# Kernel optimization log

Measured on AMD Instinct MI355X. Metric: run time of the kernel, lower is better.

The kernel has to match this reference:

```python
import jax, jax.numpy as jnp
import numpy as np

DIM = 512

def setup_inputs() -> dict:
    key = jax.random.key(0)
    k1, k2, k3 = jax.random.split(key, 3)
    context = jax.random.normal(k1, (64, 1024, DIM), dtype=jnp.float32)
    query = jax.random.normal(k2, (64, 128, DIM), dtype=jnp.float32)
    # nn.Linear(3*dim, 1, bias=False) weight, flattened to a (3*dim,) vector
    w0 = jax.random.normal(k3, (3 * DIM,), dtype=jnp.float32) * (1.0 / np.sqrt(3 * DIM))
    return {"context": context, "query": query, "w0": w0}

def reference(context, query, w0):
    # Trilinear similarity: sim[b,i,j] = w_c.c_i + w_q.q_j + w_m.(c_i*q_j)
    # (equivalent to Linear(concat([c, q, c*q])) without materializing the concat)
    d = context.shape[-1]
    wc, wq, wm = w0[:d], w0[d:2 * d], w0[2 * d:]
    sim = (context @ wc)[:, :, None] \
        + (query @ wq)[:, None, :] \
        + jnp.einsum('bid,bjd->bij', context * wm, query)  # (B, ctx, q)
    # Original: softmax over trailing dim of size 1 -> all ones (faithful to the bug)
    S = jnp.ones_like(sim)                 # (B, ctx, q)
    SS = jax.nn.softmax(sim, axis=1)       # softmax over context dim
    A = S @ query                          # (B, ctx, d)
    B = S @ jnp.swapaxes(SS, 1, 2) @ context  # (B, ctx, d)
    return (A, B)
```

## Files before the change

### kernel.cpp

```cpp
#include <hip/hip_runtime.h>
#include <hip/hip_bf16.h>

#define NB   64
#define NC   1024
#define NQ   128
#define DIMD 512
#define BK   64
#define NKC  (DIMD / BK)
#define LDK  (BK + 8)
#define TM   128
#define NTILE (NC / TM)

using short8  = __attribute__((ext_vector_type(8))) short;
using short4v = __attribute__((ext_vector_type(4))) short;
using f32x4   = __attribute__((ext_vector_type(4))) float;
typedef __fp16 half2v __attribute__((ext_vector_type(2)));

__device__ inline float dot4(float4 a, float4 b) {
    return a.x * b.x + a.y * b.y + a.z * b.z + a.w * b.w;
}

__global__ __launch_bounds__(256) void gemm_stats(
    const float* __restrict__ ctx, const float* __restrict__ qry,
    const float* __restrict__ w0, float* __restrict__ stats,
    unsigned short* __restrict__ eh)
{
    __shared__ __attribute__((aligned(16))) short As[TM][LDK];
    __shared__ __attribute__((aligned(16))) short Bs[NQ][LDK];
    __shared__ __attribute__((aligned(16))) float w0L[3 * DIMD];
    __shared__ float cwL[TM], qwL[NQ];
    __shared__ float sL[2][NQ];

    const int tid  = threadIdx.x;
    const int b    = blockIdx.x;
    const int bt   = blockIdx.y;
    const int i0   = bt * TM;
    const int w    = tid >> 6;
    const int lane = tid & 63;
    const int wr   = w >> 1, wcg = w & 1;
    const int RB   = wr * 64, CB = wcg * 64;
    const int n16  = lane & 15, qd = lane >> 4;

    for (int idx = tid; idx < 3 * DIMD; idx += 256) w0L[idx] = w0[idx];

    f32x4 acc[4][4];
#pragma unroll
    for (int ri = 0; ri < 4; ri++)
#pragma unroll
        for (int ci = 0; ci < 4; ci++)
#pragma unroll
            for (int e = 0; e < 4; e++) acc[ri][ci][e] = 0.f;

    const int col4  = n16 * 4;
    const int srow0 = w * 32 + qd;
    const float* cBase = ctx + ((size_t)(b * NC + i0 + srow0)) * DIMD + col4;
    const float* qBase = qry + ((size_t)(b * NQ + srow0)) * DIMD + col4;
    float cwp[8], qwp[8];
#pragma unroll
    for (int u = 0; u < 8; u++) { cwp[u] = 0.f; qwp[u] = 0.f; }

    for (int kc = 0; kc < NKC; kc++) {
        const int k0 = kc * BK;
        __syncthreads();
        float4 wcv = *(const float4*)&w0L[k0 + col4];
        float4 wqv = *(const float4*)&w0L[DIMD + k0 + col4];
        float4 wmv = *(const float4*)&w0L[2 * DIMD + k0 + col4];
#pragma unroll
        for (int u = 0; u < 8; u++) {
            const int row = w * 32 + u * 4 + qd;
            float4 v = *(const float4*)(cBase + k0 + (size_t)u * 4 * DIMD);
            cwp[u] += dot4(v, wcv);
            union { __hip_bfloat162 h[2]; short4v s; } pc;
            pc.h[0] = __float22bfloat162_rn(make_float2(v.x * wmv.x, v.y * wmv.y));
            pc.h[1] = __float22bfloat162_rn(make_float2(v.z * wmv.z, v.w * wmv.w));
            *(short4v*)&As[row][col4] = pc.s;

            float4 q = *(const float4*)(qBase + k0 + (size_t)u * 4 * DIMD);
            qwp[u] += dot4(q, wqv);
            union { __hip_bfloat162 h[2]; short4v s; } pq;
            pq.h[0] = __float22bfloat162_rn(make_float2(q.x, q.y));
            pq.h[1] = __float22bfloat162_rn(make_float2(q.z, q.w));
            *(short4v*)&Bs[row][col4] = pq.s;
        }
        __syncthreads();
#pragma unroll
        for (int ks = 0; ks < BK / 32; ks++) {
            const int kb = ks * 32 + qd * 8;
            short8 af[4], bfr[4];
#pragma unroll
            for (int ri = 0; ri < 4; ri++) af[ri] = *(const short8*)&As[RB + ri * 16 + n16][kb];
#pragma unroll
            for (int ci = 0; ci < 4; ci++) bfr[ci] = *(const short8*)&Bs[CB + ci * 16 + n16][kb];
#pragma unroll
            for (int ri = 0; ri < 4; ri++)
#pragma unroll
                for (int ci = 0; ci < 4; ci++)
                    acc[ri][ci] = __builtin_amdgcn_mfma_f32_16x16x32_bf16(
                        af[ri], bfr[ci], acc[ri][ci], 0, 0, 0);
        }
    }

#pragma unroll
    for (int u = 0; u < 8; u++) {
        float c = cwp[u], q = qwp[u];
#pragma unroll
        for (int off = 1; off < 16; off <<= 1) {
            c += __shfl_xor(c, off);
            q += __shfl_xor(q, off);
        }
        if (n16 == 0) {
            const int row = w * 32 + u * 4 + qd;
            cwL[row] = c; qwL[row] = q;
        }
    }
    __syncthreads();

#pragma unroll
    for (int ci = 0; ci < 4; ci++) {
        const int col = CB + ci * 16 + n16;
        const float qwv = qwL[col];
        unsigned short* eCol = eh + ((size_t)(b * NTILE + bt) * NQ + col) * TM;
        float s = 0.f;
#pragma unroll
        for (int ri = 0; ri < 4; ri++) {
            const int rbase = RB + ri * 16 + qd * 4;
            float e0 = __expf(acc[ri][ci][0] + cwL[rbase + 0] + qwv);
            float e1 = __expf(acc[ri][ci][1] + cwL[rbase + 1] + qwv);
            float e2 = __expf(acc[ri][ci][2] + cwL[rbase + 2] + qwv);
            float e3 = __expf(acc[ri][ci][3] + cwL[rbase + 3] + qwv);
            half2v h01 = __builtin_amdgcn_cvt_pkrtz(e0, e1);
            half2v h23 = __builtin_amdgcn_cvt_pkrtz(e2, e3);
            s += (float)h01[0] + (float)h01[1] + (float)h23[0] + (float)h23[1];
            uint2 pk;
            pk.x = __builtin_bit_cast(unsigned, h01);
            pk.y = __builtin_bit_cast(unsigned, h23);
            *(uint2*)&eCol[rbase] = pk;
        }
        s += __shfl_xor(s, 16);
        s += __shfl_xor(s, 32);
        if (qd == 0) sL[wr][col] = s;
    }
    __syncthreads();
    if (tid < NQ)
        stats[(size_t)(b * NTILE + bt) * NQ + tid] = sL[0][tid] + sL[1][tid];
}

__global__ __launch_bounds__(256) void rb2(
    const float* __restrict__ ctx, const float* __restrict__ qry,
    const unsigned short* __restrict__ eh, const float* __restrict__ stats,
    float* __restrict__ bpart, float* __restrict__ arow)
{
    __shared__ __attribute__((aligned(16))) unsigned short eL[NQ * TM];
    __shared__ float izL[NQ];
    __shared__ float rpart[2][TM];
    __shared__ float rfin[TM];
    __shared__ float qL[4][64];

    const int tid = threadIdx.x;
    const int b = blockIdx.x, bt = blockIdx.y;
    const int i0 = bt * TM;

    if (tid < NQ) {
        float ssum = 0.f;
#pragma unroll
        for (int t8 = 0; t8 < NTILE; t8++)
            ssum += stats[(size_t)(b * NTILE + t8) * NQ + tid];
        izL[tid] = 1.0f / ssum;
    }
    const unsigned short* tileSrc = eh + (size_t)(b * NTILE + bt) * NQ * TM;
#pragma unroll
    for (int it = 0; it < 8; it++) {
        const int idx = (tid + it * 256) * 8;
        *(uint4*)&eL[idx] = *(const uint4*)&tileSrc[idx];
    }
    __syncthreads();

    const int i = tid & 127, jh = tid >> 7;
    float r = 0.f;
    for (int j2 = 0; j2 < 64; j2++) {
        const int j = jh * 64 + j2;
        __fp16 hv = __builtin_bit_cast(__fp16, eL[j * TM + i]);
        r += (float)hv * izL[j];
    }
    rpart[jh][i] = r;
    __syncthreads();
    if (tid < TM) rfin[tid] = rpart[0][tid] + rpart[1][tid];
    __syncthreads();

    const int d0 = tid * 2;
    float bx = 0.f, by = 0.f;
    const float* cb2 = ctx + ((size_t)b * NC + i0) * DIMD + d0;
    for (int ii = 0; ii < TM; ii++) {
        float  rv = rfin[ii];
        float2 cv = *(const float2*)(cb2 + (size_t)ii * DIMD);
        bx += rv * cv.x; by += rv * cv.y;
    }
    float* bp = bpart + (size_t)(b * NTILE + bt) * DIMD + d0;
    bp[0] = bx; bp[1] = by;

    const int dcol = tid & 63, rgrp = tid >> 6;
    float qs = 0.f;
    const float* qb = qry + (size_t)b * NQ * DIMD + bt * 64 + dcol;
    for (int t = 0; t < 32; t++)
        qs += qb[(size_t)(t * 4 + rgrp) * DIMD];
    qL[rgrp][dcol] = qs;
    __syncthreads();
    if (tid < 64)
        arow[(size_t)b * DIMD + bt * 64 + tid] =
            qL[0][tid] + qL[1][tid] + qL[2][tid] + qL[3][tid];
}

__global__ void broadcast_out(const float* __restrict__ arow, const float* __restrict__ bpart,
                              float* __restrict__ out)
{
    const int b = blockIdx.x, ic = blockIdx.y;
    const int t = threadIdx.x;
    const int half = t >> 7;
    const int l = t & 127;
    const int d0 = l * 4;
    f32x4 val;
    if (half == 0) {
        val = *(const f32x4*)&arow[(size_t)b * DIMD + d0];
    } else {
        val[0] = val[1] = val[2] = val[3] = 0.f;
        for (int t8 = 0; t8 < NTILE; t8++) {
            f32x4 v = *(const f32x4*)&bpart[(size_t)(b * NTILE + t8) * DIMD + d0];
            val[0] += v[0]; val[1] += v[1]; val[2] += v[2]; val[3] += v[3];
        }
    }
    size_t base = (size_t)half * ((size_t)NB * NC * DIMD)
                + ((size_t)b * NC + (size_t)ic * 32) * DIMD + d0;
    for (int i = 0; i < 32; i++)
        __builtin_nontemporal_store(val, (f32x4*)&out[base + (size_t)i * DIMD]);
}

extern "C" void kernel_launch(void* const* d_in, const int* in_sizes, int n_in,
                              void* d_out, int out_size, void* d_ws, size_t ws_size,
                              hipStream_t stream)
{
    const float* ctx = (const float*)d_in[0];
    const float* qry = (const float*)d_in[1];
    const float* w0  = (const float*)d_in[2];
    float* out = (float*)d_out;
    float* ws  = (float*)d_ws;

    float* stats = ws;
    float* arow  = ws + 65536;
    float* bpart = ws + 98304;
    unsigned short* eh = (unsigned short*)(ws + 360448);

    gemm_stats<<<dim3(NB, NTILE), 256, 0, stream>>>(ctx, qry, w0, stats, eh);
    rb2<<<dim3(NB, NTILE), 256, 0, stream>>>(ctx, qry, eh, stats, bpart, arow);
    broadcast_out<<<dim3(NB, 32), 256, 0, stream>>>(arow, bpart, out);
}
```

Before: 416.1 us.

## Split bf16 prep into separate kernel and double-buffer GEMM via direct global-to-LDS loads

New measurement: 425.7 us. +2.3%, slower.

```diff
diff --git a/kernel.cpp b/kernel.cpp
--- a/kernel.cpp
+++ b/kernel.cpp
@@ -7,7 +7,6 @@
 #define DIMD 512
 #define BK   64
 #define NKC  (DIMD / BK)
-#define LDK  (BK + 8)
 #define TM   128
 #define NTILE (NC / TM)
 
@@ -20,14 +19,73 @@
     return a.x * b.x + a.y * b.y + a.z * b.z + a.w * b.w;
 }
 
-__global__ __launch_bounds__(256) void gemm_stats(
+__device__ inline short4v pack_bf16(float a, float b, float c, float d) {
+    union { __hip_bfloat162 h[2]; short4v s; } p;
+    p.h[0] = __float22bfloat162_rn(make_float2(a, b));
+    p.h[1] = __float22bfloat162_rn(make_float2(c, d));
+    return p.s;
+}
+
+__device__ __forceinline__ void glds16(const void* g, void* l) {
+    __builtin_amdgcn_global_load_lds(
+        (const __attribute__((address_space(1))) unsigned int*)g,
+        (__attribute__((address_space(3))) unsigned int*)l,
+        16, 0, 0);
+}
+
+__global__ __launch_bounds__(256) void prep(
     const float* __restrict__ ctx, const float* __restrict__ qry,
-    const float* __restrict__ w0, float* __restrict__ stats,
-    unsigned short* __restrict__ eh)
-{
-    __shared__ __attribute__((aligned(16))) short As[TM][LDK];
-    __shared__ __attribute__((aligned(16))) short Bs[NQ][LDK];
-    __shared__ __attribute__((aligned(16))) float w0L[3 * DIMD];
+    const float* __restrict__ w0,
+    unsigned short* __restrict__ cm, unsigned short* __restrict__ qm,
+    float* __restrict__ cw, float* __restrict__ qw)
+{
+    const int wv   = threadIdx.x >> 6;
+    const int lane = threadIdx.x & 63;
+    const int gid  = blockIdx.x * 4 + wv;
+    const int d0   = lane * 8;
+    const int NCTX = NB * NC;
+
+    if (gid < NCTX) {
+        const float* src = ctx + (size_t)gid * DIMD + d0;
+        float4 v0 = *(const float4*)src;
+        float4 v1 = *(const float4*)(src + 4);
+        float4 m0 = *(const float4*)&w0[2 * DIMD + d0];
+        float4 m1 = *(const float4*)&w0[2 * DIMD + d0 + 4];
+        float4 c0 = *(const float4*)&w0[d0];
+        float4 c1 = *(const float4*)&w0[d0 + 4];
+        union { short4v h[2]; short8 v; } pk;
+        pk.h[0] = pack_bf16(v0.x * m0.x, v0.y * m0.y, v0.z * m0.z, v0.w * m0.w);
+        pk.h[1] = pack_bf16(v1.x * m1.x, v1.y * m1.y, v1.z * m1.z, v1.w * m1.w);
+        *(short8*)(cm + (size_t)gid * DIMD + d0) = pk.v;
+        float s = dot4(v0, c0) + dot4(v1, c1);
+#pragma unroll
+        for (int off = 1; off < 64; off <<= 1) s += __shfl_xor(s, off);
+        if (lane == 0) cw[gid] = s;
+    } else {
+        const int j = gid - NCTX;
+        const float* src = qry + (size_t)j * DIMD + d0;
+        float4 v0 = *(const float4*)src;
+        float4 v1 = *(const float4*)(src + 4);
+        float4 q0 = *(const float4*)&w0[DIMD + d0];
+        float4 q1 = *(const float4*)&w0[DIMD + d0 + 4];
+        union { short4v h[2]; short8 v; } pk;
+        pk.h[0] = pack_bf16(v0.x, v0.y, v0.z, v0.w);
+        pk.h[1] = pack_bf16(v1.x, v1.y, v1.z, v1.w);
+        *(short8*)(qm + (size_t)j * DIMD + d0) = pk.v;
+        float s = dot4(v0, q0) + dot4(v1, q1);
+#pragma unroll
+        for (int off = 1; off < 64; off <<= 1) s += __shfl_xor(s, off);
+        if (lane == 0) qw[j] = s;
+    }
+}
+
+__global__ __launch_bounds__(256) void gemm_e(
+    const unsigned short* __restrict__ cm, const unsigned short* __restrict__ qm,
+    const float* __restrict__ cw, const float* __restrict__ qw,
+    float* __restrict__ stats, unsigned short* __restrict__ eh)
+{
+    __shared__ __attribute__((aligned(16))) unsigned short Abuf[2][TM][64];
+    __shared__ __attribute__((aligned(16))) unsigned short Bbuf[2][NQ][64];
     __shared__ float cwL[TM], qwL[NQ];
     __shared__ float sL[2][NQ];
 
@@ -40,8 +98,16 @@
     const int wr   = w >> 1, wcg = w & 1;
     const int RB   = wr * 64, CB = wcg * 64;
     const int n16  = lane & 15, qd = lane >> 4;
-
-    for (int idx = tid; idx < 3 * DIMD; idx += 256) w0L[idx] = w0[idx];
+    const int x7   = n16 & 7;
+
+    if (tid < TM) cwL[tid] = cw[(size_t)b * NC + i0 + tid];
+    else          qwL[tid - TM] = qw[(size_t)b * NQ + (tid - TM)];
+
+    const int rl  = lane >> 3;
+    const int cc  = lane & 7;
+    const int csw = cc ^ rl;
+    const unsigned short* aSrc = cm + ((size_t)b * NC + i0 + w * 32 + rl) * DIMD + csw * 8;
+    const unsigned short* bSrc = qm + ((size_t)b * NQ +      w * 32 + rl) * DIMD + csw * 8;
 
     f32x4 acc[4][4];
 #pragma unroll
@@ -51,46 +117,36 @@
 #pragma unroll
             for (int e = 0; e < 4; e++) acc[ri][ci][e] = 0.f;
 
-    const int col4  = n16 * 4;
-    const int srow0 = w * 32 + qd;
-    const float* cBase = ctx + ((size_t)(b * NC + i0 + srow0)) * DIMD + col4;
-    const float* qBase = qry + ((size_t)(b * NQ + srow0)) * DIMD + col4;
-    float cwp[8], qwp[8];
-#pragma unroll
-    for (int u = 0; u < 8; u++) { cwp[u] = 0.f; qwp[u] = 0.f; }
+    auto stage = [&](int buf, int kc) {
+        const int kof = kc * 64;
+#pragma unroll
+        for (int i = 0; i < 4; i++) {
+            glds16(aSrc + (size_t)i * 8 * DIMD + kof, (void*)&Abuf[buf][w * 32 + i * 8][0]);
+            glds16(bSrc + (size_t)i * 8 * DIMD + kof, (void*)&Bbuf[buf][w * 32 + i * 8][0]);
+        }
+    };
+
+    stage(0, 0);
+    __syncthreads();
 
     for (int kc = 0; kc < NKC; kc++) {
-        const int k0 = kc * BK;
-        __syncthreads();
-        float4 wcv = *(const float4*)&w0L[k0 + col4];
-        float4 wqv = *(const float4*)&w0L[DIMD + k0 + col4];
-        float4 wmv = *(const float4*)&w0L[2 * DIMD + k0 + col4];
-#pragma unroll
-        for (int u = 0; u < 8; u++) {
-            const int row = w * 32 + u * 4 + qd;
-            float4 v = *(const float4*)(cBase + k0 + (size_t)u * 4 * DIMD);
-            cwp[u] += dot4(v, wcv);
-            union { __hip_bfloat162 h[2]; short4v s; } pc;
-            pc.h[0] = __float22bfloat162_rn(make_float2(v.x * wmv.x, v.y * wmv.y));
-            pc.h[1] = __float22bfloat162_rn(make_float2(v.z * wmv.z, v.w * wmv.w));
-            *(short4v*)&As[row][col4] = pc.s;
-
-            float4 q = *(const float4*)(qBase + k0 + (size_t)u * 4 * DIMD);
-            qwp[u] += dot4(q, wqv);
-            union { __hip_bfloat162 h[2]; short4v s; } pq;
-            pq.h[0] = __float22bfloat162_rn(make_float2(q.x, q.y));
-            pq.h[1] = __float22bfloat162_rn(make_float2(q.z, q.w));
-            *(short4v*)&Bs[row][col4] = pq.s;
-        }
-        __syncthreads();
-#pragma unroll
-        for (int ks = 0; ks < BK / 32; ks++) {
-            const int kb = ks * 32 + qd * 8;
+        const int cur = kc & 1;
+        if (kc + 1 < NKC) stage(cur ^ 1, kc + 1);
+#pragma unroll
+        for (int ks = 0; ks < 2; ks++) {
             short8 af[4], bfr[4];
 #pragma unroll
-            for (int ri = 0; ri < 4; ri++) af[ri] = *(const short8*)&As[RB + ri * 16 + n16][kb];
-#pragma unroll
-            for (int ci = 0; ci < 4; ci++) bfr[ci] = *(const short8*)&Bs[CB + ci * 16 + n16][kb];
+            for (int ri = 0; ri < 4; ri++) {
+                const int rA = RB + ri * 16 + n16;
+                const int p  = (ks * 4 + qd) ^ x7;
+                af[ri] = *(const short8*)&Abuf[cur][rA][p * 8];
+            }
+#pragma unroll
+            for (int ci = 0; ci < 4; ci++) {
+                const int rB = CB + ci * 16 + n16;
+                const int p  = (ks * 4 + qd) ^ x7;
+                bfr[ci] = *(const short8*)&Bbuf[cur][rB][p * 8];
+            }
 #pragma unroll
             for (int ri = 0; ri < 4; ri++)
 #pragma unroll
@@ -98,22 +154,8 @@
                     acc[ri][ci] = __builtin_amdgcn_mfma_f32_16x16x32_bf16(
                         af[ri], bfr[ci], acc[ri][ci], 0, 0, 0);
         }
-    }
-
-#pragma unroll
-    for (int u = 0; u < 8; u++) {
-        float c = cwp[u], q = qwp[u];
-#pragma unroll
-        for (int off = 1; off < 16; off <<= 1) {
-            c += __shfl_xor(c, off);
-            q += __shfl_xor(q, off);
-        }
-        if (n16 == 0) {
-            const int row = w * 32 + u * 4 + qd;
-            cwL[row] = c; qwL[row] = q;
-        }
-    }
-    __syncthreads();
+        __syncthreads();
+    }
 
 #pragma unroll
     for (int ci = 0; ci < 4; ci++) {
@@ -154,6 +196,7 @@
     __shared__ float izL[NQ];
     __shared__ float rpart[2][TM];
     __shared__ float rfin[TM];
+    __shared__ float bH[2][DIMD];
     __shared__ float qL[4][64];
 
     const int tid = threadIdx.x;
@@ -187,16 +230,25 @@
     if (tid < TM) rfin[tid] = rpart[0][tid] + rpart[1][tid];
     __syncthreads();
 
-    const int d0 = tid * 2;
-    float bx = 0.f, by = 0.f;
-    const float* cb2 = ctx + ((size_t)b * NC + i0) * DIMD + d0;
-    for (int ii = 0; ii < TM; ii++) {
-        float  rv = rfin[ii];
-        float2 cv = *(const float2*)(cb2 + (size_t)ii * DIMD);
-        bx += rv * cv.x; by += rv * cv.y;
-    }
-    float* bp = bpart + (size_t)(b * NTILE + bt) * DIMD + d0;
-    bp[0] = bx; bp[1] = by;
+    const int dq = (tid & 127) * 4;
+    const int rh = tid >> 7;
+    f32x4 ba = {0.f, 0.f, 0.f, 0.f};
+    const float* cb4 = ctx + ((size_t)b * NC + i0 + rh * 64) * DIMD + dq;
+#pragma unroll 4
+    for (int ii = 0; ii < 64; ii++) {
+        float rv = rfin[rh * 64 + ii];
+        f32x4 cv = *(const f32x4*)(cb4 + (size_t)ii * DIMD);
+        ba += rv * cv;
+    }
+    *(f32x4*)&bH[rh][dq] = ba;
+    __syncthreads();
+    if (tid < 128) {
+        const int d4 = tid * 4;
+        f32x4 r0 = *(const f32x4*)&bH[0][d4];
+        f32x4 r1 = *(const f32x4*)&bH[1][d4];
+        f32x4 sum = r0 + r1;
+        *(f32x4*)&bpart[(size_t)(b * NTILE + bt) * DIMD + d4] = sum;
+    }
 
     const int dcol = tid & 63, rgrp = tid >> 6;
     float qs = 0.f;
@@ -244,12 +296,17 @@
     float* out = (float*)d_out;
     float* ws  = (float*)d_ws;
 
-    float* stats = ws;
-    float* arow  = ws + 65536;
-    float* bpart = ws + 98304;
-    unsigned short* eh = (unsigned short*)(ws + 360448);
-
-    gemm_stats<<<dim3(NB, NTILE), 256, 0, stream>>>(ctx, qry, w0, stats, eh);
+    unsigned short* cm = (unsigned short*)ws;
+    unsigned short* qm = (unsigned short*)(ws + 16777216);
+    float* cw    = ws + 18874368;
+    float* qw    = ws + 18939904;
+    float* stats = ws + 18948096;
+    float* arow  = ws + 19013632;
+    float* bpart = ws + 19046400;
+    unsigned short* eh = (unsigned short*)(ws + 19308544);
+
+    prep<<<dim3((NB * NC + NB * NQ) / 4), 256, 0, stream>>>(ctx, qry, w0, cm, qm, cw, qw);
+    gemm_e<<<dim3(NB, NTILE), 256, 0, stream>>>(cm, qm, cw, qw, stats, eh);
     rb2<<<dim3(NB, NTILE), 256, 0, stream>>>(ctx, qry, eh, stats, bpart, arow);
     broadcast_out<<<dim3(NB, 32), 256, 0, stream>>>(arow, bpart, out);
 }
```

## Remap block order for XCD locality, batch global loads, vectorize context reduction

Applied to the files above, without the earlier changes.

New measurement: 414.0 us. Within noise of the previous version (-0.5%).

```diff
diff --git a/kernel.cpp b/kernel.cpp
--- a/kernel.cpp
+++ b/kernel.cpp
@@ -32,8 +32,10 @@
     __shared__ float sL[2][NQ];
 
     const int tid  = threadIdx.x;
-    const int b    = blockIdx.x;
-    const int bt   = blockIdx.y;
+    const int bid  = blockIdx.x;
+    const int orig = (bid & 7) * 64 + (bid >> 3);
+    const int b    = orig >> 3;
+    const int bt   = orig & 7;
     const int i0   = bt * TM;
     const int w    = tid >> 6;
     const int lane = tid & 63;
@@ -65,21 +67,26 @@
         float4 wcv = *(const float4*)&w0L[k0 + col4];
         float4 wqv = *(const float4*)&w0L[DIMD + k0 + col4];
         float4 wmv = *(const float4*)&w0L[2 * DIMD + k0 + col4];
+
+        float4 cv[8], qv[8];
+#pragma unroll
+        for (int u = 0; u < 8; u++) {
+            cv[u] = *(const float4*)(cBase + k0 + (size_t)u * 4 * DIMD);
+            qv[u] = *(const float4*)(qBase + k0 + (size_t)u * 4 * DIMD);
+        }
 #pragma unroll
         for (int u = 0; u < 8; u++) {
             const int row = w * 32 + u * 4 + qd;
-            float4 v = *(const float4*)(cBase + k0 + (size_t)u * 4 * DIMD);
-            cwp[u] += dot4(v, wcv);
+            cwp[u] += dot4(cv[u], wcv);
             union { __hip_bfloat162 h[2]; short4v s; } pc;
-            pc.h[0] = __float22bfloat162_rn(make_float2(v.x * wmv.x, v.y * wmv.y));
-            pc.h[1] = __float22bfloat162_rn(make_float2(v.z * wmv.z, v.w * wmv.w));
+            pc.h[0] = __float22bfloat162_rn(make_float2(cv[u].x * wmv.x, cv[u].y * wmv.y));
+            pc.h[1] = __float22bfloat162_rn(make_float2(cv[u].z * wmv.z, cv[u].w * wmv.w));
             *(short4v*)&As[row][col4] = pc.s;
 
-            float4 q = *(const float4*)(qBase + k0 + (size_t)u * 4 * DIMD);
-            qwp[u] += dot4(q, wqv);
+            qwp[u] += dot4(qv[u], wqv);
             union { __hip_bfloat162 h[2]; short4v s; } pq;
-            pq.h[0] = __float22bfloat162_rn(make_float2(q.x, q.y));
-            pq.h[1] = __float22bfloat162_rn(make_float2(q.z, q.w));
+            pq.h[0] = __float22bfloat162_rn(make_float2(qv[u].x, qv[u].y));
+            pq.h[1] = __float22bfloat162_rn(make_float2(qv[u].z, qv[u].w));
             *(short4v*)&Bs[row][col4] = pq.s;
         }
         __syncthreads();
@@ -154,11 +161,15 @@
     __shared__ float izL[NQ];
     __shared__ float rpart[2][TM];
     __shared__ float rfin[TM];
+    __shared__ float bH[2][DIMD];
     __shared__ float qL[4][64];
 
-    const int tid = threadIdx.x;
-    const int b = blockIdx.x, bt = blockIdx.y;
-    const int i0 = bt * TM;
+    const int tid  = threadIdx.x;
+    const int bid  = blockIdx.x;
+    const int orig = (bid & 7) * 64 + (bid >> 3);
+    const int b    = orig >> 3;
+    const int bt   = orig & 7;
+    const int i0   = bt * TM;
 
     if (tid < NQ) {
         float ssum = 0.f;
@@ -187,16 +198,25 @@
     if (tid < TM) rfin[tid] = rpart[0][tid] + rpart[1][tid];
     __syncthreads();
 
-    const int d0 = tid * 2;
-    float bx = 0.f, by = 0.f;
-    const float* cb2 = ctx + ((size_t)b * NC + i0) * DIMD + d0;
-    for (int ii = 0; ii < TM; ii++) {
-        float  rv = rfin[ii];
-        float2 cv = *(const float2*)(cb2 + (size_t)ii * DIMD);
-        bx += rv * cv.x; by += rv * cv.y;
-    }
-    float* bp = bpart + (size_t)(b * NTILE + bt) * DIMD + d0;
-    bp[0] = bx; bp[1] = by;
+    const int dq = (tid & 127) * 4;
+    const int rh = tid >> 7;
+    f32x4 ba = {0.f, 0.f, 0.f, 0.f};
+    const float* cb4 = ctx + ((size_t)b * NC + i0 + rh * 64) * DIMD + dq;
+#pragma unroll 4
+    for (int ii = 0; ii < 64; ii++) {
+        float rv = rfin[rh * 64 + ii];
+        f32x4 cv = *(const f32x4*)(cb4 + (size_t)ii * DIMD);
+        ba += rv * cv;
+    }
+    *(f32x4*)&bH[rh][dq] = ba;
+    __syncthreads();
+    if (tid < 128) {
+        const int d4 = tid * 4;
+        f32x4 r0 = *(const f32x4*)&bH[0][d4];
+        f32x4 r1 = *(const f32x4*)&bH[1][d4];
+        f32x4 sum = r0 + r1;
+        *(f32x4*)&bpart[(size_t)(b * NTILE + bt) * DIMD + d4] = sum;
+    }
 
     const int dcol = tid & 63, rgrp = tid >> 6;
     float qs = 0.f;
@@ -249,7 +269,7 @@
     float* bpart = ws + 98304;
     unsigned short* eh = (unsigned short*)(ws + 360448);
 
-    gemm_stats<<<dim3(NB, NTILE), 256, 0, stream>>>(ctx, qry, w0, stats, eh);
-    rb2<<<dim3(NB, NTILE), 256, 0, stream>>>(ctx, qry, eh, stats, bpart, arow);
+    gemm_stats<<<dim3(NB * NTILE), 256, 0, stream>>>(ctx, qry, w0, stats, eh);
+    rb2<<<dim3(NB * NTILE), 256, 0, stream>>>(ctx, qry, eh, stats, bpart, arow);
     broadcast_out<<<dim3(NB, 32), 256, 0, stream>>>(arow, bpart, out);
 }
```
